# Performance work log

Hardware: AMD Instinct MI355X
Metric: run time of the kernel (lower is better)

The kernel has to match this reference:

```python
import jax, jax.numpy as jnp
import numpy as np

NUM_CLASSES = 1000
FEAT = 192
HID = 256
TOTAL_NODES = 8192  # 16 images * 512 patches, kNN is global (no batch vector in source)


def _knn_idx(x, k):
    # squared euclidean distances, top-k smallest (self-loop included: d(i,i)=0)
    sq = jnp.sum(x * x, axis=-1)                       # [N]
    d = sq[:, None] + sq[None, :] - 2.0 * (x @ x.T)    # [N, N]
    _, idx = jax.lax.top_k(-d, k)                      # [N, k] neighbor indices per node
    return idx


def _sage_conv(x, idx, w_l, b_l, w_r):
    # PyG SAGEConv (mean aggr): lin_l(mean_j x_j) + lin_r(x_i); bias on lin_l
    agg = jnp.mean(x[idx], axis=1)                     # [N, C_in] mean over k neighbors
    return agg @ w_l + b_l + x @ w_r


def setup_inputs() -> dict:
    key = jax.random.key(0)
    ks = jax.random.split(key, 8)
    s = lambda fi, fo: (2.0 / (fi + fo)) ** 0.5
    return {
        "x": jax.random.normal(ks[0], (TOTAL_NODES, FEAT), dtype=jnp.float32),
        "w_l0": jax.random.normal(ks[1], (FEAT, HID), jnp.float32) * s(FEAT, HID),
        "b_l0": jnp.zeros((HID,), jnp.float32),
        "w_r0": jax.random.normal(ks[2], (FEAT, HID), jnp.float32) * s(FEAT, HID),
        "w_l1": jax.random.normal(ks[3], (HID, HID), jnp.float32) * s(HID, HID),
        "b_l1": jnp.zeros((HID,), jnp.float32),
        "w_r1": jax.random.normal(ks[4], (HID, HID), jnp.float32) * s(HID, HID),
        "w_l2": jax.random.normal(ks[5], (HID, NUM_CLASSES), jnp.float32) * s(HID, NUM_CLASSES),
        "b_l2": jnp.zeros((NUM_CLASSES,), jnp.float32),
        "w_r2": jax.random.normal(ks[6], (HID, NUM_CLASSES), jnp.float32) * s(HID, NUM_CLASSES),
        "k": 9,
        "batch_size": 16,
    }


def reference(x, w_l0, b_l0, w_r0, w_l1, b_l1, w_r1, w_l2, b_l2, w_r2, k, batch_size):
    idx = _knn_idx(x, k)  # graph built once from input features, reused by all layers
    h = jax.nn.relu(_sage_conv(x, idx, w_l0, b_l0, w_r0))
    h = jax.nn.relu(_sage_conv(h, idx, w_l1, b_l1, w_r1))
    h = jax.nn.relu(_sage_conv(h, idx, w_l2, b_l2, w_r2))
    # global_mean_pool with batch = arange(B).repeat_interleave(N/B): equal-size segments
    h = h.reshape(batch_size, -1, h.shape[-1]).mean(axis=1)  # [B, num_classes]
    return h
```

## Files before the change

### kernel.cpp

```cpp
#include <hip/hip_runtime.h>

#define NN   8192
#define FEAT 192
#define HID  256
#define NCLS 1000
#define KNN  9
#define NPP  512
#define NIMG 16
#define KD   192
#define KL0  384
#define NCB  32
#define FINF 3.402823466e38f

typedef unsigned short ushort_t;
typedef unsigned int uint_t;
typedef __attribute__((ext_vector_type(8))) __bf16 bf16x8;
typedef __attribute__((ext_vector_type(4))) float f32x4;

#define ASYNC16(gptr, lptr)                                                  \
  __builtin_amdgcn_global_load_lds(                                          \
      (const __attribute__((address_space(1))) void*)(gptr),                 \
      (__attribute__((address_space(3))) void*)(lptr), 16, 0, 0)

#define MFMA(a, b, c) __builtin_amdgcn_mfma_f32_16x16x32_bf16((a), (b), (c), 0, 0, 0)

__device__ __forceinline__ ushort_t f2bf_rne(float f) {
  unsigned u = __float_as_uint(f);
  u += 0x7FFF + ((u >> 16) & 1);
  return (ushort_t)(u >> 16);
}
__device__ __forceinline__ float bf2f(ushort_t u) {
  return __uint_as_float((unsigned)u << 16);
}

__device__ __forceinline__ float packf(float v, int col) {
  return __uint_as_float((__float_as_uint(v) & 0xFFFFE000u) | (uint_t)col);
}

__device__ __forceinline__ float fmed3(float a, float b, float c) {
  float d;
  asm("v_med3_f32 %0, %1, %2, %3" : "=v"(d) : "v"(a), "v"(b), "v"(c));
  return d;
}

__device__ __forceinline__ void bubble9f(float (&tk)[KNN], float k) {
#pragma unroll
  for (int p = KNN - 1; p > 0; --p) tk[p] = fmed3(tk[p - 1], tk[p], k);
  tk[0] = fminf(tk[0], k);
}

__global__ __launch_bounds__(256) void k_prep(
    const float* __restrict__ x, float* __restrict__ sq,
    ushort_t* __restrict__ xs,
    const float* __restrict__ w_l0, const float* __restrict__ w_r0,
    const float* __restrict__ w_l1, const float* __restrict__ w_r1,
    const float* __restrict__ w_l2, const float* __restrict__ w_r2,
    ushort_t* __restrict__ WT0, ushort_t* __restrict__ WT1,
    ushort_t* __restrict__ WT2, float* __restrict__ out) {
  const int blk = blockIdx.x, t = threadIdx.x;
  if (blk < 2048) {
    int wid  = (blk * 256 + t) >> 6;
    int lane = t & 63;
    const float* row = x + (size_t)wid * FEAT;
    ushort_t* xr = xs + (size_t)wid * KD;
    float s = 0.f;
#pragma unroll
    for (int f0 = 0; f0 < FEAT; f0 += 64) {
      int f = f0 + lane;
      float v = row[f];
      s += v * v;
      xr[f] = f2bf_rne(v);
    }
#pragma unroll
    for (int off = 32; off > 0; off >>= 1) s += __shfl_down(s, off);
    if (lane == 0) sq[wid] = s;
    return;
  }
  int i = (blk - 2048) * 256 + t;
  if (i < NIMG * NCLS) out[i] = 0.f;
  if (i < 98304) {
    int n = i / 384, k = i - n * 384;
    float v = (k < 192) ? w_l0[k * 256 + n] : w_r0[(k - 192) * 256 + n];
    WT0[i] = f2bf_rne(v);
  } else if (i < 98304 + 131072) {
    int j = i - 98304;
    int n = j / 512, k = j - n * 512;
    float v = (k < 256) ? w_l1[k * 256 + n] : w_r1[(k - 256) * 256 + n];
    WT1[j] = f2bf_rne(v);
  } else {
    int j = i - (98304 + 131072);
    int n = j / 512, k = j - n * 512;
    float v = 0.f;
    if (n < NCLS)
      v = (k < 256) ? w_l2[k * NCLS + n] : w_r2[(k - 256) * NCLS + n];
    WT2[j] = f2bf_rne(v);
  }
}

__global__ __launch_bounds__(256, 4) void k_dist_topk(
    const ushort_t* __restrict__ xs, const float* __restrict__ sq,
    float* __restrict__ cand) {
  __shared__ __align__(16) char smem[24576];
  ushort_t* As = (ushort_t*)smem;
  ushort_t* Bs = (ushort_t*)(smem + 8192);
  float*    Ms = (float*)(smem + 19456);

  const int t    = threadIdx.x;
  const int lane = t & 63;
  const int w    = t >> 6;
  const int l15  = lane & 15, lq = lane >> 4;
  const int rowStart = blockIdx.y * 128;
  const int colBase  = blockIdx.x * 256;
  const int mrow = (w >> 1) * 64;
  const int ncol = (w & 1) * 64;

  const int m0 = w * 128 + lane;
  const int r0 = m0 >> 2, r1 = r0 + 16;
  const int g0 = m0 & 3;
  const int gs0 = g0 ^ (r0 & 3);
  const int gs1 = g0 ^ (r1 & 3);
  const ushort_t* gA0 = xs + (size_t)(rowStart + r0) * KD + gs0 * 8;
  const ushort_t* gA1 = xs + (size_t)(rowStart + r1) * KD + gs1 * 8;
  ushort_t* lA = As + w * 1024;
  ushort_t* lB = Bs + w * 1024;

  const int pg = (lq ^ (l15 & 3)) * 8;
  int aoff[4], boff[4];
#pragma unroll
  for (int ti = 0; ti < 4; ++ti) aoff[ti] = (mrow + ti * 16 + l15) * 32 + pg;
#pragma unroll
  for (int tj = 0; tj < 4; ++tj) boff[tj] = (ncol + tj * 16 + l15) * 32 + pg;

  float tk[KNN];
#pragma unroll
  for (int n = 0; n < KNN; ++n) tk[n] = FINF;

  float* Ew = (float*)smem + w * (64 * 19);

#pragma unroll 1
  for (int ct = 0; ct < 2; ++ct) {
    const int colStart = colBase + ct * 128;
    const ushort_t* gB0 = xs + (size_t)(colStart + r0) * KD + gs0 * 8;
    const ushort_t* gB1 = xs + (size_t)(colStart + r1) * KD + gs1 * 8;

    f32x4 c00 = {}, c01 = {}, c02 = {}, c03 = {};
    f32x4 c10 = {}, c11 = {}, c12 = {}, c13 = {};
    f32x4 c20 = {}, c21 = {}, c22 = {}, c23 = {};
    f32x4 c30 = {}, c31 = {}, c32 = {}, c33 = {};

#pragma unroll 1
    for (int kt = 0; kt < 6; ++kt) {
      const int k0 = kt * 32;
      ASYNC16(gA0 + k0, lA);
      ASYNC16(gA1 + k0, lA + 512);
      ASYNC16(gB0 + k0, lB);
      ASYNC16(gB1 + k0, lB + 512);
      __syncthreads();
      bf16x8 a0 = *(const bf16x8*)(As + aoff[0]);
      bf16x8 a1 = *(const bf16x8*)(As + aoff[1]);
      bf16x8 a2 = *(const bf16x8*)(As + aoff[2]);
      bf16x8 a3 = *(const bf16x8*)(As + aoff[3]);
      bf16x8 b0 = *(const bf16x8*)(Bs + boff[0]);
      bf16x8 b1 = *(const bf16x8*)(Bs + boff[1]);
      bf16x8 b2 = *(const bf16x8*)(Bs + boff[2]);
      bf16x8 b3 = *(const bf16x8*)(Bs + boff[3]);
      c00 = MFMA(a0, b0, c00); c01 = MFMA(a0, b1, c01);
      c02 = MFMA(a0, b2, c02); c03 = MFMA(a0, b3, c03);
      c10 = MFMA(a1, b0, c10); c11 = MFMA(a1, b1, c11);
      c12 = MFMA(a1, b2, c12); c13 = MFMA(a1, b3, c13);
      c20 = MFMA(a2, b0, c20); c21 = MFMA(a2, b1, c21);
      c22 = MFMA(a2, b2, c22); c23 = MFMA(a2, b3, c23);
      c30 = MFMA(a3, b0, c30); c31 = MFMA(a3, b1, c31);
      c32 = MFMA(a3, b2, c32); c33 = MFMA(a3, b3, c33);
      __syncthreads();
    }

#define EPI_ROW(TI, CV)                                                      \
  do {                                                                       \
    f32x4 v_ = (CV);                                                         \
    Ew[((TI) * 16 + lq * 4 + 0) * 19 + l15] =                                \
        packf(fmaf(-2.0f, v_.x, sqv), mycol);                                \
    Ew[((TI) * 16 + lq * 4 + 1) * 19 + l15] =                                \
        packf(fmaf(-2.0f, v_.y, sqv), mycol);                                \
    Ew[((TI) * 16 + lq * 4 + 2) * 19 + l15] =                                \
        packf(fmaf(-2.0f, v_.z, sqv), mycol);                                \
    Ew[((TI) * 16 + lq * 4 + 3) * 19 + l15] =                                \
        packf(fmaf(-2.0f, v_.w, sqv), mycol);                                \
  } while (0)

#define EPI_TILE(TJ, C0, C1, C2, C3)                                         \
  do {                                                                       \
    int mycol = colStart + ncol + (TJ) * 16 + l15;                           \
    float sqv = sq[mycol];                                                   \
    EPI_ROW(0, C0); EPI_ROW(1, C1); EPI_ROW(2, C2); EPI_ROW(3, C3);          \
    _Pragma("unroll")                                                        \
    for (int c = 0; c < 16; ++c) bubble9f(tk, Ew[lane * 19 + c]);            \
  } while (0)

    EPI_TILE(0, c00, c10, c20, c30);
    EPI_TILE(1, c01, c11, c21, c31);
    EPI_TILE(2, c02, c12, c22, c32);
    EPI_TILE(3, c03, c13, c23, c33);

    __syncthreads();
  }

  if (w & 1) {
#pragma unroll
    for (int n = 0; n < KNN; ++n) Ms[(mrow + lane) * 10 + n] = tk[n];
  }
  __syncthreads();
  if (!(w & 1)) {
#pragma unroll
    for (int n = 0; n < KNN; ++n) bubble9f(tk, Ms[(mrow + lane) * 10 + n]);
    size_t base =
        (((size_t)(rowStart + mrow + lane)) * NCB + blockIdx.x) * KNN;
#pragma unroll
    for (int n = 0; n < KNN; ++n) cand[base + n] = tk[n];
  }
}

__global__ __launch_bounds__(256) void k_reduce_gather(
    const float* __restrict__ cand, const float* __restrict__ x,
    int* __restrict__ idx, ushort_t* __restrict__ Ab0) {
  int wid  = (blockIdx.x * 256 + threadIdx.x) >> 6;
  int lane = threadIdx.x & 63;
  if (wid >= NN) return;
  const float* cv = cand + (size_t)wid * (NCB * KNN);
  float tk[KNN];
#pragma unroll
  for (int n = 0; n < KNN; ++n) tk[n] = FINF;
#pragma unroll
  for (int m = 0; m < 4; ++m) bubble9f(tk, cv[lane + 64 * m]);
  bubble9f(tk, (lane < 32) ? cv[lane + 256] : FINF);

  int nb[KNN];
  for (int r = 0; r < KNN; ++r) {
    float bm = tk[0];
#pragma unroll
    for (int off = 32; off > 0; off >>= 1)
      bm = fminf(bm, __shfl_xor(bm, off));
    if (tk[0] == bm) {
#pragma unroll
      for (int p = 0; p < KNN - 1; ++p) tk[p] = tk[p + 1];
      tk[KNN - 1] = FINF;
    }
    nb[r] = (int)(__float_as_uint(bm) & 0x1FFFu);
    if (lane == 0) idx[wid * KNN + r] = nb[r];
  }

#pragma unroll
  for (int f0 = 0; f0 < FEAT; f0 += 64) {
    int f = f0 + lane;
    float s = 0.f;
#pragma unroll
    for (int n = 0; n < KNN; ++n) s += x[(size_t)nb[n] * FEAT + f];
    Ab0[(size_t)wid * KL0 + f]        = f2bf_rne(s * (1.0f / KNN));
    Ab0[(size_t)wid * KL0 + FEAT + f] = f2bf_rne(x[(size_t)wid * FEAT + f]);
  }
}

__global__ __launch_bounds__(256) void k_gather_h(
    const ushort_t* __restrict__ hsrc, const int* __restrict__ idx,
    ushort_t* __restrict__ adst) {
  const int t = threadIdx.x;
  const int lane = t & 63, w = t >> 6;
  const int r  = (blockIdx.x * 4 + w) * 2 + (lane >> 5);
  const int cl = (lane & 31) * 8;
  int nb[KNN];
#pragma unroll
  for (int n = 0; n < KNN; ++n) nb[n] = idx[r * KNN + n];
  float s[8] = {};
#pragma unroll
  for (int n = 0; n < KNN; ++n) {
    uint4 v = *(const uint4*)(hsrc + (size_t)nb[n] * 512 + cl);
    s[0] += __uint_as_float(v.x << 16); s[1] += __uint_as_float(v.x & 0xFFFF0000u);
    s[2] += __uint_as_float(v.y << 16); s[3] += __uint_as_float(v.y & 0xFFFF0000u);
    s[4] += __uint_as_float(v.z << 16); s[5] += __uint_as_float(v.z & 0xFFFF0000u);
    s[6] += __uint_as_float(v.w << 16); s[7] += __uint_as_float(v.w & 0xFFFF0000u);
  }
  uint4 o;
  o.x = (uint_t)f2bf_rne(s[0] * (1.0f / KNN)) |
        ((uint_t)f2bf_rne(s[1] * (1.0f / KNN)) << 16);
  o.y = (uint_t)f2bf_rne(s[2] * (1.0f / KNN)) |
        ((uint_t)f2bf_rne(s[3] * (1.0f / KNN)) << 16);
  o.z = (uint_t)f2bf_rne(s[4] * (1.0f / KNN)) |
        ((uint_t)f2bf_rne(s[5] * (1.0f / KNN)) << 16);
  o.w = (uint_t)f2bf_rne(s[6] * (1.0f / KNN)) |
        ((uint_t)f2bf_rne(s[7] * (1.0f / KNN)) << 16);
  *(uint4*)(adst + (size_t)r * 512 + cl) = o;
}

__global__ __launch_bounds__(256) void k_sage64(
    const ushort_t* __restrict__ Ab, const ushort_t* __restrict__ WT,
    const float* __restrict__ bias, ushort_t* __restrict__ hdst, int KT) {
  __shared__ __align__(16) char smem[16384];
  ushort_t* As = (ushort_t*)smem;
  ushort_t* Bs = (ushort_t*)(smem + 8192);
  const int blk = blockIdx.x;
  const int t = threadIdx.x;
  const int lane = t & 63, w = t >> 6;
  const int l15 = lane & 15, lq = lane >> 4;
  const int rowStart = (blk >> 2) * 64, colStart = (blk & 3) * 64;
  const int mrow = (w >> 1) * 32, ncol = (w & 1) * 32;

  const int rA = t >> 2, g = t & 3;
  const int gs = g ^ (rA & 3);
  const ushort_t* gA = Ab + (size_t)(rowStart + rA) * KT + gs * 8;
  const ushort_t* gB = WT + (size_t)(colStart + rA) * KT + gs * 8;
  ushort_t* lA = As + w * 512;
  ushort_t* lB = Bs + w * 512;

  const int pg = (lq ^ (l15 & 3)) * 8;
  const int aoff0 = (mrow + l15) * 32 + pg, aoff1 = (mrow + 16 + l15) * 32 + pg;
  const int boff0 = (ncol + l15) * 32 + pg, boff1 = (ncol + 16 + l15) * 32 + pg;

  f32x4 c00 = {}, c01 = {}, c10 = {}, c11 = {};
  const int nkt = KT >> 6;
#pragma unroll 1
  for (int kt = 0; kt < nkt; ++kt) {
    const int k0 = kt * 64;
    ASYNC16(gA + k0, lA);
    ASYNC16(gA + k0 + 32, lA + 2048);
    ASYNC16(gB + k0, lB);
    ASYNC16(gB + k0 + 32, lB + 2048);
    __syncthreads();
    bf16x8 a0 = *(const bf16x8*)(As + aoff0);
    bf16x8 a1 = *(const bf16x8*)(As + aoff1);
    bf16x8 b0 = *(const bf16x8*)(Bs + boff0);
    bf16x8 b1 = *(const bf16x8*)(Bs + boff1);
    c00 = MFMA(a0, b0, c00); c01 = MFMA(a0, b1, c01);
    c10 = MFMA(a1, b0, c10); c11 = MFMA(a1, b1, c11);
    bf16x8 a0p = *(const bf16x8*)(As + 2048 + aoff0);
    bf16x8 a1p = *(const bf16x8*)(As + 2048 + aoff1);
    bf16x8 b0p = *(const bf16x8*)(Bs + 2048 + boff0);
    bf16x8 b1p = *(const bf16x8*)(Bs + 2048 + boff1);
    c00 = MFMA(a0p, b0p, c00); c01 = MFMA(a0p, b1p, c01);
    c10 = MFMA(a1p, b0p, c10); c11 = MFMA(a1p, b1p, c11);
    __syncthreads();
  }

  const float bv0 = bias[colStart + ncol + l15];
  const float bv1 = bias[colStart + ncol + 16 + l15];
#define S64_ST(TI, TJ, CV, BV)                                               \
  do {                                                                       \
    f32x4 v_ = (CV);                                                         \
    int col_ = colStart + ncol + (TJ) * 16 + l15;                            \
    size_t rb_ = (size_t)(rowStart + mrow + (TI) * 16 + lq * 4);             \
    hdst[(rb_ + 0) * 512 + col_] = f2bf_rne(fmaxf(v_.x + (BV), 0.f));        \
    hdst[(rb_ + 1) * 512 + col_] = f2bf_rne(fmaxf(v_.y + (BV), 0.f));        \
    hdst[(rb_ + 2) * 512 + col_] = f2bf_rne(fmaxf(v_.z + (BV), 0.f));        \
    hdst[(rb_ + 3) * 512 + col_] = f2bf_rne(fmaxf(v_.w + (BV), 0.f));        \
  } while (0)
  S64_ST(0, 0, c00, bv0); S64_ST(0, 1, c01, bv1);
  S64_ST(1, 0, c10, bv0); S64_ST(1, 1, c11, bv1);
}

__global__ __launch_bounds__(256, 2) void k_sage128_pool(
    const ushort_t* __restrict__ Ab, const ushort_t* __restrict__ WT,
    const float* __restrict__ bias, float* __restrict__ out) {
  __shared__ __align__(16) char smem[32768];
  ushort_t* As = (ushort_t*)smem;
  ushort_t* Bs = (ushort_t*)(smem + 16384);
  __shared__ float Ps[2][128];

  const int t    = threadIdx.x;
  const int lane = t & 63;
  const int w    = t >> 6;
  const int l15  = lane & 15, lq = lane >> 4;
  const int rowStart = blockIdx.y * 128;
  const int colStart = blockIdx.x * 128;
  const int mrow = (w >> 1) * 64;
  const int ncol = (w & 1) * 64;
  const int KT = 512;

  const int rA0 = t >> 2, rA1 = rA0 + 64;
  const int g = t & 3;
  const int gsA0 = g ^ (rA0 & 3), gsA1 = g ^ (rA1 & 3);
  const ushort_t* gA0 = Ab + (size_t)(rowStart + rA0) * KT + gsA0 * 8;
  const ushort_t* gA1 = Ab + (size_t)(rowStart + rA1) * KT + gsA1 * 8;
  const ushort_t* gB0 = WT + (size_t)(colStart + rA0) * KT + gsA0 * 8;
  const ushort_t* gB1 = WT + (size_t)(colStart + rA1) * KT + gsA1 * 8;
  ushort_t* lA0 = As + w * 512;
  ushort_t* lA1 = As + 2048 + w * 512;
  ushort_t* lB0 = Bs + w * 512;
  ushort_t* lB1 = Bs + 2048 + w * 512;

  const int pg = (lq ^ (l15 & 3)) * 8;
  int aoff[4], boff[4];
#pragma unroll
  for (int ti = 0; ti < 4; ++ti) aoff[ti] = (mrow + ti * 16 + l15) * 32 + pg;
#pragma unroll
  for (int tj = 0; tj < 4; ++tj) boff[tj] = (ncol + tj * 16 + l15) * 32 + pg;

  f32x4 c00 = {}, c01 = {}, c02 = {}, c03 = {};
  f32x4 c10 = {}, c11 = {}, c12 = {}, c13 = {};
  f32x4 c20 = {}, c21 = {}, c22 = {}, c23 = {};
  f32x4 c30 = {}, c31 = {}, c32 = {}, c33 = {};

#define POOL_MFMA_PANEL(OFS)                                                 \
  do {                                                                       \
    bf16x8 a0 = *(const bf16x8*)(As + (OFS) + aoff[0]);                      \
    bf16x8 a1 = *(const bf16x8*)(As + (OFS) + aoff[1]);                      \
    bf16x8 a2 = *(const bf16x8*)(As + (OFS) + aoff[2]);                      \
    bf16x8 a3 = *(const bf16x8*)(As + (OFS) + aoff[3]);                      \
    bf16x8 b0v = *(const bf16x8*)(Bs + (OFS) + boff[0]);                     \
    bf16x8 b1v = *(const bf16x8*)(Bs + (OFS) + boff[1]);                     \
    bf16x8 b2v = *(const bf16x8*)(Bs + (OFS) + boff[2]);                     \
    bf16x8 b3v = *(const bf16x8*)(Bs + (OFS) + boff[3]);                     \
    c00 = MFMA(a0, b0v, c00); c01 = MFMA(a0, b1v, c01);                      \
    c02 = MFMA(a0, b2v, c02); c03 = MFMA(a0, b3v, c03);                      \
    c10 = MFMA(a1, b0v, c10); c11 = MFMA(a1, b1v, c11);                      \
    c12 = MFMA(a1, b2v, c12); c13 = MFMA(a1, b3v, c13);                      \
    c20 = MFMA(a2, b0v, c20); c21 = MFMA(a2, b1v, c21);                      \
    c22 = MFMA(a2, b2v, c22); c23 = MFMA(a2, b3v, c23);                      \
    c30 = MFMA(a3, b0v, c30); c31 = MFMA(a3, b1v, c31);                      \
    c32 = MFMA(a3, b2v, c32); c33 = MFMA(a3, b3v, c33);                      \
  } while (0)

#pragma unroll 1
  for (int kt = 0; kt < 8; ++kt) {
    const int k0 = kt * 64;
    ASYNC16(gA0 + k0, lA0);
    ASYNC16(gA1 + k0, lA1);
    ASYNC16(gA0 + k0 + 32, lA0 + 4096);
    ASYNC16(gA1 + k0 + 32, lA1 + 4096);
    ASYNC16(gB0 + k0, lB0);
    ASYNC16(gB1 + k0, lB1);
    ASYNC16(gB0 + k0 + 32, lB0 + 4096);
    ASYNC16(gB1 + k0 + 32, lB1 + 4096);
    __syncthreads();
    POOL_MFMA_PANEL(0);
    POOL_MFMA_PANEL(4096);
    __syncthreads();
  }

#define P_ACC(CV)                                                            \
  (fmaxf((CV).x + bv_, 0.f) + fmaxf((CV).y + bv_, 0.f) +                     \
   fmaxf((CV).z + bv_, 0.f) + fmaxf((CV).w + bv_, 0.f))

#define POOL_COL(TJ, C0, C1, C2, C3)                                         \
  do {                                                                       \
    int col_ = colStart + ncol + (TJ) * 16 + l15;                            \
    float bv_ = (col_ < NCLS) ? bias[col_] : 0.f;                            \
    float s_ = P_ACC(C0) + P_ACC(C1) + P_ACC(C2) + P_ACC(C3);                \
    s_ += __shfl_xor(s_, 16);                                                \
    s_ += __shfl_xor(s_, 32);                                                \
    if (lq == 0) Ps[w >> 1][ncol + (TJ) * 16 + l15] = s_;                    \
  } while (0)

  POOL_COL(0, c00, c10, c20, c30);
  POOL_COL(1, c01, c11, c21, c31);
  POOL_COL(2, c02, c12, c22, c32);
  POOL_COL(3, c03, c13, c23, c33);

  __syncthreads();
  if (t < 128) {
    int col = colStart + t;
    if (col < NCLS) {
      float s = Ps[0][t] + Ps[1][t];
      int img = rowStart / NPP;
      atomicAdd(out + (size_t)img * NCLS + col, s * (1.0f / NPP));
    }
  }
}

extern "C" void kernel_launch(void* const* d_in, const int* in_sizes, int n_in,
                              void* d_out, int out_size, void* d_ws,
                              size_t ws_size, hipStream_t stream) {
  const float* x    = (const float*)d_in[0];
  const float* w_l0 = (const float*)d_in[1];
  const float* b_l0 = (const float*)d_in[2];
  const float* w_r0 = (const float*)d_in[3];
  const float* w_l1 = (const float*)d_in[4];
  const float* b_l1 = (const float*)d_in[5];
  const float* w_r1 = (const float*)d_in[6];
  const float* w_l2 = (const float*)d_in[7];
  const float* b_l2 = (const float*)d_in[8];
  const float* w_r2 = (const float*)d_in[9];
  float* out = (float*)d_out;

  char* ws = (char*)d_ws;
  float*    sq   = (float*)(ws);
  int*      idx  = (int*)(ws + 32768);
  float*    cand = (float*)(ws + 327680);
  ushort_t* xs   = (ushort_t*)(ws + 19202048);
  ushort_t* Ab0  = (ushort_t*)(ws + 22347776);
  ushort_t* WT0  = (ushort_t*)(ws + 28639232);
  ushort_t* WT1  = (ushort_t*)(ws + 28835840);
  ushort_t* WT2  = (ushort_t*)(ws + 29097984);
  ushort_t* Ab1  = (ushort_t*)(ws + 327680);
  ushort_t* Ab2  = (ushort_t*)(ws + 8716288);

  k_prep<<<4992, 256, 0, stream>>>(x, sq, xs, w_l0, w_r0, w_l1, w_r1,
                                   w_l2, w_r2, WT0, WT1, WT2, out);
  k_dist_topk<<<dim3(NCB, 64), 256, 0, stream>>>(xs, sq, cand);
  k_reduce_gather<<<2048, 256, 0, stream>>>(cand, x, idx, Ab0);
  k_sage64<<<512, 256, 0, stream>>>(Ab0, WT0, b_l0, Ab1 + 256, KL0);
  k_gather_h<<<1024, 256, 0, stream>>>(Ab1 + 256, idx, Ab1);
  k_sage64<<<512, 256, 0, stream>>>(Ab1, WT1, b_l1, Ab2 + 256, 512);
  k_gather_h<<<1024, 256, 0, stream>>>(Ab2 + 256, idx, Ab2);
  k_sage128_pool<<<dim3(8, 64), 256, 0, stream>>>(Ab2, WT2, b_l2, out);
}
```

Before: 182.0 us.

## Double-buffer distance GEMM loads and fuse layer-1 neighbor gather into SAGE GEMM

The distance/top-k kernel now double-buffers its LDS tiles, issuing the next k-slice's async loads before computing on the current one and dropping one barrier per iteration. A new kernel fuses the layer-1 neighbor mean aggregation into the SAGE GEMM. It gathers and averages neighbor rows into LDS, then runs the GEMM, which removes one launch and the round trip of the aggregated half through global memory. In exchange, LDS use per block rises, which may lower occupancy, and the gather is repeated by each of the four column blocks.

New measurement: 189.1 us. 1.04x slower.

```diff
diff --git a/kernel.cpp b/kernel.cpp
--- a/kernel.cpp
+++ b/kernel.cpp
@@ -100,10 +100,10 @@
 __global__ __launch_bounds__(256, 4) void k_dist_topk(
     const ushort_t* __restrict__ xs, const float* __restrict__ sq,
     float* __restrict__ cand) {
-  __shared__ __align__(16) char smem[24576];
+  __shared__ __align__(16) char smem[37888];
   ushort_t* As = (ushort_t*)smem;
-  ushort_t* Bs = (ushort_t*)(smem + 8192);
-  float*    Ms = (float*)(smem + 19456);
+  ushort_t* Bs = As + 4096;
+  float*    Ms = (float*)(smem + 32768);
 
   const int t    = threadIdx.x;
   const int lane = t & 63;
@@ -148,22 +148,31 @@
     f32x4 c20 = {}, c21 = {}, c22 = {}, c23 = {};
     f32x4 c30 = {}, c31 = {}, c32 = {}, c33 = {};
 
+    ASYNC16(gA0, lA);
+    ASYNC16(gA1, lA + 512);
+    ASYNC16(gB0, lB);
+    ASYNC16(gB1, lB + 512);
+
 #pragma unroll 1
     for (int kt = 0; kt < 6; ++kt) {
-      const int k0 = kt * 32;
-      ASYNC16(gA0 + k0, lA);
-      ASYNC16(gA1 + k0, lA + 512);
-      ASYNC16(gB0 + k0, lB);
-      ASYNC16(gB1 + k0, lB + 512);
+      const int bo = (kt & 1) * 8192;
       __syncthreads();
-      bf16x8 a0 = *(const bf16x8*)(As + aoff[0]);
-      bf16x8 a1 = *(const bf16x8*)(As + aoff[1]);
-      bf16x8 a2 = *(const bf16x8*)(As + aoff[2]);
-      bf16x8 a3 = *(const bf16x8*)(As + aoff[3]);
-      bf16x8 b0 = *(const bf16x8*)(Bs + boff[0]);
-      bf16x8 b1 = *(const bf16x8*)(Bs + boff[1]);
-      bf16x8 b2 = *(const bf16x8*)(Bs + boff[2]);
-      bf16x8 b3 = *(const bf16x8*)(Bs + boff[3]);
+      if (kt < 5) {
+        const int no = ((kt & 1) ^ 1) * 8192;
+        const int k1 = (kt + 1) * 32;
+        ASYNC16(gA0 + k1, lA + no);
+        ASYNC16(gA1 + k1, lA + no + 512);
+        ASYNC16(gB0 + k1, lB + no);
+        ASYNC16(gB1 + k1, lB + no + 512);
+      }
+      bf16x8 a0 = *(const bf16x8*)(As + bo + aoff[0]);
+      bf16x8 a1 = *(const bf16x8*)(As + bo + aoff[1]);
+      bf16x8 a2 = *(const bf16x8*)(As + bo + aoff[2]);
+      bf16x8 a3 = *(const bf16x8*)(As + bo + aoff[3]);
+      bf16x8 b0 = *(const bf16x8*)(Bs + bo + boff[0]);
+      bf16x8 b1 = *(const bf16x8*)(Bs + bo + boff[1]);
+      bf16x8 b2 = *(const bf16x8*)(Bs + bo + boff[2]);
+      bf16x8 b3 = *(const bf16x8*)(Bs + bo + boff[3]);
       c00 = MFMA(a0, b0, c00); c01 = MFMA(a0, b1, c01);
       c02 = MFMA(a0, b2, c02); c03 = MFMA(a0, b3, c03);
       c10 = MFMA(a1, b0, c10); c11 = MFMA(a1, b1, c11);
@@ -172,8 +181,8 @@
       c22 = MFMA(a2, b2, c22); c23 = MFMA(a2, b3, c23);
       c30 = MFMA(a3, b0, c30); c31 = MFMA(a3, b1, c31);
       c32 = MFMA(a3, b2, c32); c33 = MFMA(a3, b3, c33);
-      __syncthreads();
     }
+    __syncthreads();
 
 #define EPI_ROW(TI, CV)                                                      \
   do {                                                                       \
@@ -352,6 +361,111 @@
     hdst[(rb_ + 2) * 512 + col_] = f2bf_rne(fmaxf(v_.z + (BV), 0.f));        \
     hdst[(rb_ + 3) * 512 + col_] = f2bf_rne(fmaxf(v_.w + (BV), 0.f));        \
   } while (0)
+  S64_ST(0, 0, c00, bv0); S64_ST(0, 1, c01, bv1);
+  S64_ST(1, 0, c10, bv0); S64_ST(1, 1, c11, bv1);
+}
+
+__global__ __launch_bounds__(256) void k_sage64g(
+    const ushort_t* __restrict__ hsrc, const int* __restrict__ idx,
+    const ushort_t* __restrict__ WT, const float* __restrict__ bias,
+    ushort_t* __restrict__ hdst) {
+  __shared__ __align__(16) char smem[50176];
+  ushort_t* Ag = (ushort_t*)smem;
+  ushort_t* As = (ushort_t*)(smem + 33792);
+  ushort_t* Bs = (ushort_t*)(smem + 41984);
+  const int blk = blockIdx.x;
+  const int t = threadIdx.x;
+  const int lane = t & 63, w = t >> 6;
+  const int l15 = lane & 15, lq = lane >> 4;
+  const int rowStart = (blk >> 2) * 64, colStart = (blk & 3) * 64;
+  const int mrow = (w >> 1) * 32, ncol = (w & 1) * 32;
+
+  {
+    const int cl = lane * 4;
+#pragma unroll 1
+    for (int rr = 0; rr < 16; ++rr) {
+      int row = rowStart + w * 16 + rr;
+      int nb[KNN];
+#pragma unroll
+      for (int n = 0; n < KNN; ++n) nb[n] = idx[row * KNN + n];
+      float s0 = 0.f, s1 = 0.f, s2 = 0.f, s3 = 0.f;
+#pragma unroll
+      for (int n = 0; n < KNN; ++n) {
+        ushort4 v = *(const ushort4*)(hsrc + (size_t)nb[n] * 512 + cl);
+        s0 += bf2f(v.x); s1 += bf2f(v.y); s2 += bf2f(v.z); s3 += bf2f(v.w);
+      }
+      ushort4 o;
+      o.x = f2bf_rne(s0 * (1.0f / KNN));
+      o.y = f2bf_rne(s1 * (1.0f / KNN));
+      o.z = f2bf_rne(s2 * (1.0f / KNN));
+      o.w = f2bf_rne(s3 * (1.0f / KNN));
+      *(ushort4*)(Ag + (w * 16 + rr) * 264 + cl) = o;
+    }
+  }
+  __syncthreads();
+
+  const int rA = t >> 2, g = t & 3;
+  const int gs = g ^ (rA & 3);
+  const ushort_t* gB  = WT + (size_t)(colStart + rA) * 512 + gs * 8;
+  const ushort_t* gAh = hsrc + (size_t)(rowStart + rA) * 512 + gs * 8;
+  ushort_t* lA = As + w * 512;
+  ushort_t* lB = Bs + w * 512;
+
+  const int pg = (lq ^ (l15 & 3)) * 8;
+  const int aoff0 = (mrow + l15) * 32 + pg, aoff1 = (mrow + 16 + l15) * 32 + pg;
+  const int boff0 = (ncol + l15) * 32 + pg, boff1 = (ncol + 16 + l15) * 32 + pg;
+  const int ga0 = (mrow + l15) * 264 + lq * 8;
+  const int ga1 = (mrow + 16 + l15) * 264 + lq * 8;
+
+  f32x4 c00 = {}, c01 = {}, c10 = {}, c11 = {};
+
+#pragma unroll 1
+  for (int kt = 0; kt < 4; ++kt) {
+    const int k0 = kt * 64;
+    ASYNC16(gB + k0, lB);
+    ASYNC16(gB + k0 + 32, lB + 2048);
+    __syncthreads();
+    bf16x8 a0 = *(const bf16x8*)(Ag + ga0 + k0);
+    bf16x8 a1 = *(const bf16x8*)(Ag + ga1 + k0);
+    bf16x8 b0 = *(const bf16x8*)(Bs + boff0);
+    bf16x8 b1 = *(const bf16x8*)(Bs + boff1);
+    c00 = MFMA(a0, b0, c00); c01 = MFMA(a0, b1, c01);
+    c10 = MFMA(a1, b0, c10); c11 = MFMA(a1, b1, c11);
+    bf16x8 a0p = *(const bf16x8*)(Ag + ga0 + k0 + 32);
+    bf16x8 a1p = *(const bf16x8*)(Ag + ga1 + k0 + 32);
+    bf16x8 b0p = *(const bf16x8*)(Bs + 2048 + boff0);
+    bf16x8 b1p = *(const bf16x8*)(Bs + 2048 + boff1);
+    c00 = MFMA(a0p, b0p, c00); c01 = MFMA(a0p, b1p, c01);
+    c10 = MFMA(a1p, b0p, c10); c11 = MFMA(a1p, b1p, c11);
+    __syncthreads();
+  }
+
+#pragma unroll 1
+  for (int kt = 4; kt < 8; ++kt) {
+    const int k0 = kt * 64;
+    const int kh = k0 - 256;
+    ASYNC16(gAh + kh, lA);
+    ASYNC16(gAh + kh + 32, lA + 2048);
+    ASYNC16(gB + k0, lB);
+    ASYNC16(gB + k0 + 32, lB + 2048);
+    __syncthreads();
+    bf16x8 a0 = *(const bf16x8*)(As + aoff0);
+    bf16x8 a1 = *(const bf16x8*)(As + aoff1);
+    bf16x8 b0 = *(const bf16x8*)(Bs + boff0);
+    bf16x8 b1 = *(const bf16x8*)(Bs + boff1);
+    c00 = MFMA(a0, b0, c00); c01 = MFMA(a0, b1, c01);
+    c10 = MFMA(a1, b0, c10); c11 = MFMA(a1, b1, c11);
+    bf16x8 a0p = *(const bf16x8*)(As + 2048 + aoff0);
+    bf16x8 a1p = *(const bf16x8*)(As + 2048 + aoff1);
+    bf16x8 b0p = *(const bf16x8*)(Bs + 2048 + boff0);
+    bf16x8 b1p = *(const bf16x8*)(Bs + 2048 + boff1);
+    c00 = MFMA(a0p, b0p, c00); c01 = MFMA(a0p, b1p, c01);
+    c10 = MFMA(a1p, b0p, c10); c11 = MFMA(a1p, b1p, c11);
+    __syncthreads();
+  }
+
+  const float bv0 = bias[colStart + ncol + l15];
+  const float bv1 = bias[colStart + ncol + 16 + l15];
   S64_ST(0, 0, c00, bv0); S64_ST(0, 1, c01, bv1);
   S64_ST(1, 0, c10, bv0); S64_ST(1, 1, c11, bv1);
 }
@@ -497,8 +611,7 @@
   k_dist_topk<<<dim3(NCB, 64), 256, 0, stream>>>(xs, sq, cand);
   k_reduce_gather<<<2048, 256, 0, stream>>>(cand, x, idx, Ab0);
   k_sage64<<<512, 256, 0, stream>>>(Ab0, WT0, b_l0, Ab1 + 256, KL0);
-  k_gather_h<<<1024, 256, 0, stream>>>(Ab1 + 256, idx, Ab1);
-  k_sage64<<<512, 256, 0, stream>>>(Ab1, WT1, b_l1, Ab2 + 256, 512);
+  k_sage64g<<<512, 256, 0, stream>>>(Ab1 + 256, idx, WT1, b_l1, Ab2 + 256);
   k_gather_h<<<1024, 256, 0, stream>>>(Ab2 + 256, idx, Ab2);
   k_sage128_pool<<<dim3(8, 64), 256, 0, stream>>>(Ab2, WT2, b_l2, out);
 }
```

## Compute full 128x256 distance tile in one K pass per block

Applied to the files above, without the earlier changes.

The distance+top-k kernel now keeps a 128x256 accumulator tile (each wave handles 64x128) instead of iterating twice over 128-column halves. Each A tile is therefore loaded once per K step rather than twice, and the per-half K loops and syncs collapse into one loop. This doubles the accumulator registers (32 f32x4 per wave), lowers the launch-bounds occupancy target from 4 to 2, and enlarges shared memory. The trade is fewer global loads and barriers against fewer resident waves to hide latency during the top-k epilogue.

After: 188.0 us. 1.03x slower.

```diff
diff --git a/kernel.cpp b/kernel.cpp
--- a/kernel.cpp
+++ b/kernel.cpp
@@ -97,13 +97,14 @@
   }
 }
 
-__global__ __launch_bounds__(256, 4) void k_dist_topk(
+__global__ __launch_bounds__(256, 2) void k_dist_topk(
     const ushort_t* __restrict__ xs, const float* __restrict__ sq,
     float* __restrict__ cand) {
-  __shared__ __align__(16) char smem[24576];
+  __shared__ __align__(16) char smem[29696];
   ushort_t* As = (ushort_t*)smem;
   ushort_t* Bs = (ushort_t*)(smem + 8192);
-  float*    Ms = (float*)(smem + 19456);
+  float*    Ms = (float*)(smem + 24576);
+  float*    Ew = (float*)smem;
 
   const int t    = threadIdx.x;
   const int lane = t & 63;
@@ -111,99 +112,113 @@
   const int l15  = lane & 15, lq = lane >> 4;
   const int rowStart = blockIdx.y * 128;
   const int colBase  = blockIdx.x * 256;
-  const int mrow = (w >> 1) * 64;
-  const int ncol = (w & 1) * 64;
-
-  const int m0 = w * 128 + lane;
-  const int r0 = m0 >> 2, r1 = r0 + 16;
-  const int g0 = m0 & 3;
-  const int gs0 = g0 ^ (r0 & 3);
-  const int gs1 = g0 ^ (r1 & 3);
-  const ushort_t* gA0 = xs + (size_t)(rowStart + r0) * KD + gs0 * 8;
-  const ushort_t* gA1 = xs + (size_t)(rowStart + r1) * KD + gs1 * 8;
-  ushort_t* lA = As + w * 1024;
-  ushort_t* lB = Bs + w * 1024;
+  const int mrow  = (w >> 1) * 64;
+  const int ncol2 = (w & 1) * 128;
+
+  const int rA = t >> 2, g = t & 3;
+  const int gsA = g ^ (rA & 3);
+  const ushort_t* gA0 = xs + (size_t)(rowStart + rA) * KD + gsA * 8;
+  const ushort_t* gA1 = xs + (size_t)(rowStart + rA + 64) * KD + gsA * 8;
+  const ushort_t* gB0 = xs + (size_t)(colBase + rA) * KD + gsA * 8;
+  const ushort_t* gB1 = xs + (size_t)(colBase + 64 + rA) * KD + gsA * 8;
+  const ushort_t* gB2 = xs + (size_t)(colBase + 128 + rA) * KD + gsA * 8;
+  const ushort_t* gB3 = xs + (size_t)(colBase + 192 + rA) * KD + gsA * 8;
+  ushort_t* lA = As + (size_t)t * 8;
+  ushort_t* lB = Bs + (size_t)t * 8;
 
   const int pg = (lq ^ (l15 & 3)) * 8;
-  int aoff[4], boff[4];
+  int aoff[4], boff[8];
 #pragma unroll
   for (int ti = 0; ti < 4; ++ti) aoff[ti] = (mrow + ti * 16 + l15) * 32 + pg;
 #pragma unroll
-  for (int tj = 0; tj < 4; ++tj) boff[tj] = (ncol + tj * 16 + l15) * 32 + pg;
+  for (int tj = 0; tj < 8; ++tj) boff[tj] = (ncol2 + tj * 16 + l15) * 32 + pg;
+
+  f32x4 c00 = {}, c01 = {}, c02 = {}, c03 = {};
+  f32x4 c04 = {}, c05 = {}, c06 = {}, c07 = {};
+  f32x4 c10 = {}, c11 = {}, c12 = {}, c13 = {};
+  f32x4 c14 = {}, c15 = {}, c16 = {}, c17 = {};
+  f32x4 c20 = {}, c21 = {}, c22 = {}, c23 = {};
+  f32x4 c24 = {}, c25 = {}, c26 = {}, c27 = {};
+  f32x4 c30 = {}, c31 = {}, c32 = {}, c33 = {};
+  f32x4 c34 = {}, c35 = {}, c36 = {}, c37 = {};
+
+#pragma unroll 1
+  for (int kt = 0; kt < 6; ++kt) {
+    const int k0 = kt * 32;
+    ASYNC16(gA0 + k0, lA);
+    ASYNC16(gA1 + k0, lA + 2048);
+    ASYNC16(gB0 + k0, lB);
+    ASYNC16(gB1 + k0, lB + 2048);
+    ASYNC16(gB2 + k0, lB + 4096);
+    ASYNC16(gB3 + k0, lB + 6144);
+    __syncthreads();
+    bf16x8 a0 = *(const bf16x8*)(As + aoff[0]);
+    bf16x8 a1 = *(const bf16x8*)(As + aoff[1]);
+    bf16x8 a2 = *(const bf16x8*)(As + aoff[2]);
+    bf16x8 a3 = *(const bf16x8*)(As + aoff[3]);
+    bf16x8 b0 = *(const bf16x8*)(Bs + boff[0]);
+    bf16x8 b1 = *(const bf16x8*)(Bs + boff[1]);
+    bf16x8 b2 = *(const bf16x8*)(Bs + boff[2]);
+    bf16x8 b3 = *(const bf16x8*)(Bs + boff[3]);
+    bf16x8 b4 = *(const bf16x8*)(Bs + boff[4]);
+    bf16x8 b5 = *(const bf16x8*)(Bs + boff[5]);
+    bf16x8 b6 = *(const bf16x8*)(Bs + boff[6]);
+    bf16x8 b7 = *(const bf16x8*)(Bs + boff[7]);
+    c00 = MFMA(a0, b0, c00); c01 = MFMA(a0, b1, c01);
+    c02 = MFMA(a0, b2, c02); c03 = MFMA(a0, b3, c03);
+    c04 = MFMA(a0, b4, c04); c05 = MFMA(a0, b5, c05);
+    c06 = MFMA(a0, b6, c06); c07 = MFMA(a0, b7, c07);
+    c10 = MFMA(a1, b0, c10); c11 = MFMA(a1, b1, c11);
+    c12 = MFMA(a1, b2, c12); c13 = MFMA(a1, b3, c13);
+    c14 = MFMA(a1, b4, c14); c15 = MFMA(a1, b5, c15);
+    c16 = MFMA(a1, b6, c16); c17 = MFMA(a1, b7, c17);
+    c20 = MFMA(a2, b0, c20); c21 = MFMA(a2, b1, c21);
+    c22 = MFMA(a2, b2, c22); c23 = MFMA(a2, b3, c23);
+    c24 = MFMA(a2, b4, c24); c25 = MFMA(a2, b5, c25);
+    c26 = MFMA(a2, b6, c26); c27 = MFMA(a2, b7, c27);
+    c30 = MFMA(a3, b0, c30); c31 = MFMA(a3, b1, c31);
+    c32 = MFMA(a3, b2, c32); c33 = MFMA(a3, b3, c33);
+    c34 = MFMA(a3, b4, c34); c35 = MFMA(a3, b5, c35);
+    c36 = MFMA(a3, b6, c36); c37 = MFMA(a3, b7, c37);
+    __syncthreads();
+  }
 
   float tk[KNN];
 #pragma unroll
   for (int n = 0; n < KNN; ++n) tk[n] = FINF;
 
-  float* Ew = (float*)smem + w * (64 * 19);
-
-#pragma unroll 1
-  for (int ct = 0; ct < 2; ++ct) {
-    const int colStart = colBase + ct * 128;
-    const ushort_t* gB0 = xs + (size_t)(colStart + r0) * KD + gs0 * 8;
-    const ushort_t* gB1 = xs + (size_t)(colStart + r1) * KD + gs1 * 8;
-
-    f32x4 c00 = {}, c01 = {}, c02 = {}, c03 = {};
-    f32x4 c10 = {}, c11 = {}, c12 = {}, c13 = {};
-    f32x4 c20 = {}, c21 = {}, c22 = {}, c23 = {};
-    f32x4 c30 = {}, c31 = {}, c32 = {}, c33 = {};
-
-#pragma unroll 1
-    for (int kt = 0; kt < 6; ++kt) {
-      const int k0 = kt * 32;
-      ASYNC16(gA0 + k0, lA);
-      ASYNC16(gA1 + k0, lA + 512);
-      ASYNC16(gB0 + k0, lB);
-      ASYNC16(gB1 + k0, lB + 512);
-      __syncthreads();
-      bf16x8 a0 = *(const bf16x8*)(As + aoff[0]);
-      bf16x8 a1 = *(const bf16x8*)(As + aoff[1]);
-      bf16x8 a2 = *(const bf16x8*)(As + aoff[2]);
-      bf16x8 a3 = *(const bf16x8*)(As + aoff[3]);
-      bf16x8 b0 = *(const bf16x8*)(Bs + boff[0]);
-      bf16x8 b1 = *(const bf16x8*)(Bs + boff[1]);
-      bf16x8 b2 = *(const bf16x8*)(Bs + boff[2]);
-      bf16x8 b3 = *(const bf16x8*)(Bs + boff[3]);
-      c00 = MFMA(a0, b0, c00); c01 = MFMA(a0, b1, c01);
-      c02 = MFMA(a0, b2, c02); c03 = MFMA(a0, b3, c03);
-      c10 = MFMA(a1, b0, c10); c11 = MFMA(a1, b1, c11);
-      c12 = MFMA(a1, b2, c12); c13 = MFMA(a1, b3, c13);
-      c20 = MFMA(a2, b0, c20); c21 = MFMA(a2, b1, c21);
-      c22 = MFMA(a2, b2, c22); c23 = MFMA(a2, b3, c23);
-      c30 = MFMA(a3, b0, c30); c31 = MFMA(a3, b1, c31);
-      c32 = MFMA(a3, b2, c32); c33 = MFMA(a3, b3, c33);
-      __syncthreads();
-    }
+  float* Ewp = Ew + w * (64 * 19);
 
 #define EPI_ROW(TI, CV)                                                      \
   do {                                                                       \
     f32x4 v_ = (CV);                                                         \
-    Ew[((TI) * 16 + lq * 4 + 0) * 19 + l15] =                                \
+    Ewp[((TI) * 16 + lq * 4 + 0) * 19 + l15] =                               \
         packf(fmaf(-2.0f, v_.x, sqv), mycol);                                \
-    Ew[((TI) * 16 + lq * 4 + 1) * 19 + l15] =                                \
+    Ewp[((TI) * 16 + lq * 4 + 1) * 19 + l15] =                               \
         packf(fmaf(-2.0f, v_.y, sqv), mycol);                                \
-    Ew[((TI) * 16 + lq * 4 + 2) * 19 + l15] =                                \
+    Ewp[((TI) * 16 + lq * 4 + 2) * 19 + l15] =                               \
         packf(fmaf(-2.0f, v_.z, sqv), mycol);                                \
-    Ew[((TI) * 16 + lq * 4 + 3) * 19 + l15] =                                \
+    Ewp[((TI) * 16 + lq * 4 + 3) * 19 + l15] =                               \
         packf(fmaf(-2.0f, v_.w, sqv), mycol);                                \
   } while (0)
 
 #define EPI_TILE(TJ, C0, C1, C2, C3)                                         \
   do {                                                                       \
-    int mycol = colStart + ncol + (TJ) * 16 + l15;                           \
+    int mycol = colBase + ncol2 + (TJ) * 16 + l15;                           \
     float sqv = sq[mycol];                                                   \
     EPI_ROW(0, C0); EPI_ROW(1, C1); EPI_ROW(2, C2); EPI_ROW(3, C3);          \
     _Pragma("unroll")                                                        \
-    for (int c = 0; c < 16; ++c) bubble9f(tk, Ew[lane * 19 + c]);            \
+    for (int c = 0; c < 16; ++c) bubble9f(tk, Ewp[lane * 19 + c]);           \
   } while (0)
 
-    EPI_TILE(0, c00, c10, c20, c30);
-    EPI_TILE(1, c01, c11, c21, c31);
-    EPI_TILE(2, c02, c12, c22, c32);
-    EPI_TILE(3, c03, c13, c23, c33);
-
-    __syncthreads();
-  }
+  EPI_TILE(0, c00, c10, c20, c30);
+  EPI_TILE(1, c01, c11, c21, c31);
+  EPI_TILE(2, c02, c12, c22, c32);
+  EPI_TILE(3, c03, c13, c23, c33);
+  EPI_TILE(4, c04, c14, c24, c34);
+  EPI_TILE(5, c05, c15, c25, c35);
+  EPI_TILE(6, c06, c16, c26, c36);
+  EPI_TILE(7, c07, c17, c27, c37);
 
   if (w & 1) {
 #pragma unroll
```
